# Optimization experiments

Measured on AMD Instinct MI355X. Metric: run time of the kernel, lower is better.

## Reference

```python
import jax, jax.numpy as jnp
import numpy as np

H = 16        # num_heads
NB = 64       # n_buckets
NH = 6        # n_hyperplanes = log2(NB)


def setup_inputs() -> dict:
    key = jax.random.key(0)
    k = jax.random.split(key, 6)
    E = 1024
    B, S = 2, 2048
    return {
        "x": jax.random.normal(k[0], (B, S, E), jnp.float32),
        "Wq": jax.random.normal(k[1], (E, E), jnp.float32) * (E ** -0.5),
        "bq": jax.random.normal(k[2], (E,), jnp.float32) * 0.02,
        "Wv": jax.random.normal(k[3], (E, E), jnp.float32) * (E ** -0.5),
        "bv": jax.random.normal(k[4], (E,), jnp.float32) * 0.02,
        "hyperplanes": jax.random.normal(k[5], (E // H + 1, NH), jnp.float32),
    }


def reference(x, Wq, bq, Wv, bv, hyperplanes):
    B, S, E = x.shape
    Dh = E // H
    # projections (torch Linear: x @ W.T + b)
    q = (x @ Wq.T + bq).reshape(B, S, H, Dh)
    v = (x @ Wv.T + bv).reshape(B, S, H, Dh)

    # LSH buckets from q: append a ones column, sign-project onto hyperplanes
    qa = jnp.concatenate([q, jnp.ones((B, S, H, 1), q.dtype)], axis=-1)  # [B,S,H,Dh+1]
    proj = jnp.einsum('bshe,en->bshn', qa, hyperplanes)
    bits = (proj >= 0).astype(jnp.int32)
    buckets = jnp.einsum('bshn,n->bsh', bits, 2 ** jnp.arange(NH, dtype=jnp.int32))  # [B,S,H]
    b_hs = buckets.transpose(0, 2, 1)  # [B,H,S]

    q = q.transpose(0, 2, 1, 3)  # [B,H,S,Dh]
    v = v.transpose(0, 2, 1, 3)

    # The original sums, over all NB buckets i, of (q with bucket-i tokens zeroed)
    # times its transpose. Closed form of that sum:
    #   sum_i (1-d[bs,i])(1-d[bt,i]) = NB - 2 + [bs == bt]
    scores = jnp.einsum('bhsd,bhtd->bhst', q, q) / jnp.sqrt(jnp.float32(E))
    same = (b_hs[:, :, :, None] == b_hs[:, :, None, :]).astype(scores.dtype)
    coeff = (NB - 2) + same
    attn = jax.nn.softmax(scores * coeff, axis=-1)  # [B,H,S,S]

    out = jnp.einsum('bhst,bhtd->bhsd', attn, v)
    return out.transpose(0, 2, 1, 3).reshape(B, S, E)
```

## Files before the change

kernel.cpp:

```cpp
#include <hip/hip_runtime.h>


typedef short short8 __attribute__((ext_vector_type(8)));
typedef float f32x4 __attribute__((ext_vector_type(4)));
typedef unsigned short us4 __attribute__((ext_vector_type(4)));

__device__ __forceinline__ float bff(unsigned short h) {
    return __uint_as_float(((unsigned int)h) << 16);
}
__device__ __forceinline__ unsigned short f2bf(float f) {
    unsigned int u = __float_as_uint(f);
    u += 0x7fffu + ((u >> 16) & 1u);
    return (unsigned short)(u >> 16);
}

__device__ __forceinline__ void glds16(const unsigned short* g, unsigned short* l) {
    __builtin_amdgcn_global_load_lds(
        (const __attribute__((address_space(1))) unsigned int*)g,
        (__attribute__((address_space(3))) unsigned int*)l, 16, 0, 0);
}

__global__ __launch_bounds__(256) void split_all(
    const float* __restrict__ x, const float* __restrict__ Wq,
    const float* __restrict__ Wv,
    unsigned short* __restrict__ xh, unsigned short* __restrict__ xl,
    unsigned short* __restrict__ Wqh, unsigned short* __restrict__ Wql,
    unsigned short* __restrict__ Wvh)
{
    const int blk = blockIdx.x;
    const float* in;
    unsigned short *hi, *lo;
    int idx;
    if (blk < 4096) {
        idx = blk * 256 + threadIdx.x; in = x; hi = xh; lo = xl;
    } else if (blk < 5120) {
        idx = (blk - 4096) * 256 + threadIdx.x; in = Wq; hi = Wqh; lo = Wql;
    } else {
        idx = (blk - 5120) * 256 + threadIdx.x; in = Wv; hi = Wvh; lo = nullptr;
    }
    const float4 v = ((const float4*)in)[idx];
    us4 h;
    h.x = f2bf(v.x); h.y = f2bf(v.y); h.z = f2bf(v.z); h.w = f2bf(v.w);
    ((us4*)hi)[idx] = h;
    if (lo) {
        us4 l;
        l.x = f2bf(v.x - bff(h.x)); l.y = f2bf(v.y - bff(h.y));
        l.z = f2bf(v.z - bff(h.z)); l.w = f2bf(v.w - bff(h.w));
        ((us4*)lo)[idx] = l;
    }
}

__global__ __launch_bounds__(256, 2) void gemm_qv(
    const unsigned short* __restrict__ xh, const unsigned short* __restrict__ xl,
    const unsigned short* __restrict__ wqh, const unsigned short* __restrict__ wql,
    const unsigned short* __restrict__ wvh,
    const float* __restrict__ bq, const float* __restrict__ bv,
    unsigned short* __restrict__ Qb, unsigned short* __restrict__ Qlo,
    unsigned short* __restrict__ Vt)
{
    __shared__ unsigned short Ah[128 * 64], Al[128 * 64];
    __shared__ unsigned short Bh[128 * 64], Bl[128 * 64];

    const int tid = threadIdx.x;
    const int w = tid >> 6, lane = tid & 63;
    const int i = lane & 15, qd = lane >> 4;
    const int l8 = lane >> 3, j = lane & 7;
    const int nw = w * 32;
    const int blk = blockIdx.x;
    const bool isq = blk < 256;

    f32x4 acc[8][2];
#pragma unroll
    for (int a = 0; a < 8; ++a)
#pragma unroll
        for (int b2 = 0; b2 < 2; ++b2) acc[a][b2] = f32x4{0.f, 0.f, 0.f, 0.f};

    const int gro = ((j ^ l8) << 3);

    if (isq) {
        const int m0 = ((blk & 7) + 8 * ((blk >> 3) & 3)) * 128;
        const int n0 = (blk >> 5) * 128;
        for (int k0 = 0; k0 < 1024; k0 += 64) {
            __syncthreads();
#pragma unroll
            for (int c = 0; c < 4; ++c) {
                const int r = w * 32 + c * 8;
                const size_t gx = (size_t)(m0 + r + l8) * 1024 + k0 + gro;
                const size_t gw = (size_t)(n0 + r + l8) * 1024 + k0 + gro;
                glds16(xh + gx, &Ah[r * 64]);
                glds16(xl + gx, &Al[r * 64]);
                glds16(wqh + gw, &Bh[r * 64]);
                glds16(wql + gw, &Bl[r * 64]);
            }
            __syncthreads();
#pragma unroll
            for (int kc = 0; kc < 2; ++kc) {
                const int ch = (((kc * 4 + qd) ^ (i & 7)) << 3);
                short8 bh2[2], bl2[2];
#pragma unroll
                for (int nn = 0; nn < 2; ++nn) {
                    bh2[nn] = *(const short8*)&Bh[(nw + nn * 16 + i) * 64 + ch];
                    bl2[nn] = *(const short8*)&Bl[(nw + nn * 16 + i) * 64 + ch];
                }
#pragma unroll
                for (int mm = 0; mm < 8; ++mm) {
                    const short8 ah = *(const short8*)&Ah[(mm * 16 + i) * 64 + ch];
                    const short8 al = *(const short8*)&Al[(mm * 16 + i) * 64 + ch];
#pragma unroll
                    for (int nn = 0; nn < 2; ++nn) {
                        acc[mm][nn] = __builtin_amdgcn_mfma_f32_16x16x32_bf16(
                            ah, bh2[nn], acc[mm][nn], 0, 0, 0);
                        acc[mm][nn] = __builtin_amdgcn_mfma_f32_16x16x32_bf16(
                            al, bh2[nn], acc[mm][nn], 0, 0, 0);
                        acc[mm][nn] = __builtin_amdgcn_mfma_f32_16x16x32_bf16(
                            ah, bl2[nn], acc[mm][nn], 0, 0, 0);
                    }
                }
            }
        }
#pragma unroll
        for (int mm = 0; mm < 8; ++mm)
#pragma unroll
            for (int nn = 0; nn < 2; ++nn)
#pragma unroll
                for (int rr = 0; rr < 4; ++rr) {
                    const int row = m0 + mm * 16 + qd * 4 + rr;
                    const int col = n0 + nw + nn * 16 + i;
                    const float v = acc[mm][nn][rr] + bq[col];
                    const unsigned short hs = f2bf(v);
                    const float lo = v - bff(hs);
                    const int b = row >> 11, s = row & 2047;
                    const int hh = col >> 6, d = col & 63;
                    const size_t oi = ((size_t)((b << 4) + hh) * 2048 + s) * 64 + d;
                    Qb[oi] = hs;
                    Qlo[oi] = f2bf(lo);
                }
    } else {
        const int b2 = blk - 256;
        const int n0 = ((b2 & 7) + 8 * ((b2 >> 3) & 3)) * 128;
        const int m0 = (b2 >> 5) * 128;
        for (int k0 = 0; k0 < 1024; k0 += 64) {
            __syncthreads();
#pragma unroll
            for (int c = 0; c < 4; ++c) {
                const int r = w * 32 + c * 8;
                glds16(wvh + (size_t)(m0 + r + l8) * 1024 + k0 + gro, &Ah[r * 64]);
                glds16(xh + (size_t)(n0 + r + l8) * 1024 + k0 + gro, &Bh[r * 64]);
            }
            __syncthreads();
#pragma unroll
            for (int kc = 0; kc < 2; ++kc) {
                const int ch = (((kc * 4 + qd) ^ (i & 7)) << 3);
                short8 bf2[2];
#pragma unroll
                for (int nn = 0; nn < 2; ++nn)
                    bf2[nn] = *(const short8*)&Bh[(nw + nn * 16 + i) * 64 + ch];
#pragma unroll
                for (int mm = 0; mm < 8; ++mm) {
                    const short8 af = *(const short8*)&Ah[(mm * 16 + i) * 64 + ch];
#pragma unroll
                    for (int nn = 0; nn < 2; ++nn)
                        acc[mm][nn] = __builtin_amdgcn_mfma_f32_16x16x32_bf16(
                            af, bf2[nn], acc[mm][nn], 0, 0, 0);
                }
            }
        }
#pragma unroll
        for (int mm = 0; mm < 8; ++mm)
#pragma unroll
            for (int nn = 0; nn < 2; ++nn)
#pragma unroll
                for (int rr = 0; rr < 4; ++rr) {
                    const int rch = m0 + mm * 16 + qd * 4 + rr;
                    const int tok = n0 + nw + nn * 16 + i;
                    const float v = acc[mm][nn][rr] + bv[rch];
                    const int b = tok >> 11, s = tok & 2047;
                    Vt[((size_t)(b * 1024 + rch)) * 2048 + s] = f2bf(v);
                }
    }
}

__global__ __launch_bounds__(256) void bucket_kernel(
    const unsigned short* __restrict__ Qb, const unsigned short* __restrict__ Qlo,
    const float* __restrict__ hp,
    int* __restrict__ buckets, float* __restrict__ rown)
{
    __shared__ float hpl[65 * 6];
    const int tid = threadIdx.x;
    if (tid < 65 * 6) hpl[tid] = hp[tid];
    __syncthreads();

    const int idx = blockIdx.x * 256 + tid;
    const unsigned short* qh = Qb + (size_t)idx * 64;
    const unsigned short* ql = Qlo + (size_t)idx * 64;

    float pj[6];
    float nrm = 0.f;
#pragma unroll
    for (int n = 0; n < 6; ++n) pj[n] = hpl[64 * 6 + n];
    for (int d8 = 0; d8 < 8; ++d8) {
        const short8 vh = *(const short8*)(qh + d8 * 8);
        const short8 vl = *(const short8*)(ql + d8 * 8);
#pragma unroll
        for (int e = 0; e < 8; ++e) {
            const float q = bff((unsigned short)vh[e]) + bff((unsigned short)vl[e]);
            nrm = fmaf(q, q, nrm);
#pragma unroll
            for (int n = 0; n < 6; ++n)
                pj[n] = fmaf(q, hpl[(d8 * 8 + e) * 6 + n], pj[n]);
        }
    }
    int bkt = 0;
#pragma unroll
    for (int n = 0; n < 6; ++n) bkt |= (pj[n] >= 0.f) << n;
    buckets[idx] = bkt;
    rown[idx] = nrm;
}

__global__ __launch_bounds__(256, 2) void attn_kernel(
    const unsigned short* __restrict__ Qb, const unsigned short* __restrict__ Qlo,
    const unsigned short* __restrict__ Vt, const int* __restrict__ bks,
    const float* __restrict__ rown, float* __restrict__ out)
{
    __shared__ unsigned short Khi[64 * 64];
    __shared__ unsigned short Klo[64 * 64];
    __shared__ unsigned short Vs[64 * 64];
    __shared__ unsigned short P[4][16 * 64];
    __shared__ float smax[4];

    const int tid = threadIdx.x;
    const int w = tid >> 6, lane = tid & 63;
    const int i = lane & 15, qd = lane >> 4;
    const int l8 = lane >> 3, j = lane & 7;
    const int bh = blockIdx.x;
    const int qbase = blockIdx.y * 128 + w * 32;

    const unsigned short* Qh = Qb + (size_t)bh * 2048 * 64;
    const unsigned short* Ql = Qlo + (size_t)bh * 2048 * 64;
    const unsigned short* Vb = Vt + (size_t)bh * 64 * 2048;
    const int* bk = bks + bh * 2048;
    const float* rnh = rown + bh * 2048;
    unsigned short* Pw = &P[w][0];

    float lm = 0.f;
    for (int t = tid; t < 2048; t += 256) lm = fmaxf(lm, rnh[t]);
#pragma unroll
    for (int msk = 1; msk < 64; msk <<= 1) lm = fmaxf(lm, __shfl_xor(lm, msk));
    if (lane == 0) smax[w] = lm;
    __syncthreads();
    const float sqM = sqrtf(fmaxf(fmaxf(smax[0], smax[1]),
                                  fmaxf(smax[2], smax[3])));

    float m2row[2][4], lrun[2][4];
    int qbr[2][4];
#pragma unroll
    for (int ms = 0; ms < 2; ++ms)
#pragma unroll
        for (int r = 0; r < 4; ++r) {
            const int row = qbase + ms * 16 + qd * 4 + r;
            m2row[ms][r] = 2.84030586f * sqrtf(rnh[row]) * sqM + 0.72134754f;
            qbr[ms][r] = bk[row];
            lrun[ms][r] = 0.f;
        }

    short8 aqh0[2], aqh1[2], aql0[2], aql1[2];
#pragma unroll
    for (int ms = 0; ms < 2; ++ms) {
        const unsigned short* qp = Qh + (size_t)(qbase + ms * 16 + i) * 64 + qd * 8;
        const unsigned short* lp = Ql + (size_t)(qbase + ms * 16 + i) * 64 + qd * 8;
        aqh0[ms] = *(const short8*)qp; aqh1[ms] = *(const short8*)(qp + 32);
        aql0[ms] = *(const short8*)lp; aql1[ms] = *(const short8*)(lp + 32);
    }

    f32x4 o[2][4];
#pragma unroll
    for (int ms = 0; ms < 2; ++ms)
#pragma unroll
        for (int d = 0; d < 4; ++d) o[ms][d] = f32x4{0.f, 0.f, 0.f, 0.f};

    for (int t0 = 0; t0 < 2048; t0 += 64) {
        __syncthreads();
#pragma unroll
        for (int c2 = 0; c2 < 2; ++c2) {
            const int r = w * 16 + c2 * 8 + l8;
            const int swz = ((j ^ l8) << 3);
            glds16(Qh + (size_t)(t0 + r) * 64 + swz, &Khi[w * 1024 + c2 * 512]);
            glds16(Ql + (size_t)(t0 + r) * 64 + swz, &Klo[w * 1024 + c2 * 512]);
            glds16(Vb + (size_t)r * 2048 + t0 + swz, &Vs[w * 1024 + c2 * 512]);
        }
        __syncthreads();

        f32x4 s[2][4];
        int kb[4];
#pragma unroll
        for (int sub = 0; sub < 4; ++sub) {
            const int kr = sub * 16 + i;
            const int sw = i & 7;
            const short8 bh0 = *(const short8*)&Khi[kr * 64 + ((qd ^ sw) << 3)];
            const short8 bh1 = *(const short8*)&Khi[kr * 64 + (((qd + 4) ^ sw) << 3)];
            const short8 bl0 = *(const short8*)&Klo[kr * 64 + ((qd ^ sw) << 3)];
            const short8 bl1 = *(const short8*)&Klo[kr * 64 + (((qd + 4) ^ sw) << 3)];
            kb[sub] = bk[t0 + kr];
#pragma unroll
            for (int ms = 0; ms < 2; ++ms) {
                f32x4 t = f32x4{0.f, 0.f, 0.f, 0.f};
                t = __builtin_amdgcn_mfma_f32_16x16x32_bf16(aqh0[ms], bh0, t, 0, 0, 0);
                t = __builtin_amdgcn_mfma_f32_16x16x32_bf16(aqh1[ms], bh1, t, 0, 0, 0);
                t = __builtin_amdgcn_mfma_f32_16x16x32_bf16(aql0[ms], bh0, t, 0, 0, 0);
                t = __builtin_amdgcn_mfma_f32_16x16x32_bf16(aql1[ms], bh1, t, 0, 0, 0);
                t = __builtin_amdgcn_mfma_f32_16x16x32_bf16(aqh0[ms], bl0, t, 0, 0, 0);
                t = __builtin_amdgcn_mfma_f32_16x16x32_bf16(aqh1[ms], bl1, t, 0, 0, 0);
                s[ms][sub] = t;
            }
        }

        short8 vb0[4], vb1[4];
#pragma unroll
        for (int dsub = 0; dsub < 4; ++dsub) {
            const int dr = dsub * 16 + i;
            const int sw = i & 7;
            vb0[dsub] = *(const short8*)&Vs[dr * 64 + ((qd ^ sw) << 3)];
            vb1[dsub] = *(const short8*)&Vs[dr * 64 + (((qd + 4) ^ sw) << 3)];
        }

#pragma unroll
        for (int ms = 0; ms < 2; ++ms) {
#pragma unroll
            for (int sub = 0; sub < 4; ++sub)
#pragma unroll
                for (int r = 0; r < 4; ++r) {
                    const float c2f = (kb[sub] == qbr[ms][r]) ? 2.84030586f
                                                              : 2.79522164f;
                    const float p = exp2f(fmaf(s[ms][sub][r], c2f, -m2row[ms][r]));
                    lrun[ms][r] += p;
                    const unsigned int pu = __float_as_uint(p);
                    const int row = qd * 4 + r, col = sub * 16 + i;
                    Pw[row * 64 + (((col >> 3) ^ (row & 7)) << 3) + (col & 7)] =
                        (unsigned short)(pu >> 16);
                }
            const short8 pa0 = *(const short8*)&Pw[i * 64 + ((qd ^ (i & 7)) << 3)];
            const short8 pa1 = *(const short8*)&Pw[i * 64 + (((qd + 4) ^ (i & 7)) << 3)];
#pragma unroll
            for (int dsub = 0; dsub < 4; ++dsub) {
                o[ms][dsub] = __builtin_amdgcn_mfma_f32_16x16x32_bf16(
                    pa0, vb0[dsub], o[ms][dsub], 0, 0, 0);
                o[ms][dsub] = __builtin_amdgcn_mfma_f32_16x16x32_bf16(
                    pa1, vb1[dsub], o[ms][dsub], 0, 0, 0);
            }
        }
    }

#pragma unroll
    for (int ms = 0; ms < 2; ++ms)
#pragma unroll
        for (int r = 0; r < 4; ++r) {
#pragma unroll
            for (int msk = 1; msk < 16; msk <<= 1)
                lrun[ms][r] += __shfl_xor(lrun[ms][r], msk);
        }
    const int b = bh >> 4, h = bh & 15;
#pragma unroll
    for (int ms = 0; ms < 2; ++ms)
#pragma unroll
        for (int dsub = 0; dsub < 4; ++dsub)
#pragma unroll
            for (int r = 0; r < 4; ++r) {
                const float v = o[ms][dsub][r] / lrun[ms][r];
                const int srow = qbase + ms * 16 + qd * 4 + r;
                out[((size_t)(b * 2048 + srow)) * 1024 + h * 64 + dsub * 16 + i] = v;
            }
}

extern "C" void kernel_launch(void* const* d_in, const int* in_sizes, int n_in,
                              void* d_out, int out_size, void* d_ws, size_t ws_size,
                              hipStream_t stream)
{
    const float* x  = (const float*)d_in[0];
    const float* Wq = (const float*)d_in[1];
    const float* bq = (const float*)d_in[2];
    const float* Wv = (const float*)d_in[3];
    const float* bv = (const float*)d_in[4];
    const float* hp = (const float*)d_in[5];
    float* out = (float*)d_out;

    char* ws = (char*)d_ws;
    const size_t MB = (size_t)1 << 20;
    unsigned short* xh  = (unsigned short*)(ws);
    unsigned short* xl  = (unsigned short*)(ws + 8 * MB);
    unsigned short* Wqh = (unsigned short*)(ws + 16 * MB);
    unsigned short* Wql = (unsigned short*)(ws + 18 * MB);
    unsigned short* Wvh = (unsigned short*)(ws + 20 * MB);
    unsigned short* Qb  = (unsigned short*)(ws + 22 * MB);
    unsigned short* Qlo = (unsigned short*)(ws + 30 * MB);
    unsigned short* Vt  = (unsigned short*)(ws + 38 * MB);
    int*        buckets = (int*)(ws + 62 * MB);
    float*         rown = (float*)(ws + 62 * MB + 256 * 1024);

    split_all<<<dim3(6144), 256, 0, stream>>>(x, Wq, Wv, xh, xl, Wqh, Wql, Wvh);
    gemm_qv<<<dim3(512), 256, 0, stream>>>(xh, xl, Wqh, Wql, Wvh, bq, bv,
                                           Qb, Qlo, Vt);
    bucket_kernel<<<dim3(256), 256, 0, stream>>>(Qb, Qlo, hp, buckets, rown);
    attn_kernel<<<dim3(32, 16), 256, 0, stream>>>(Qb, Qlo, Vt, buckets, rown, out);
}
```

Baseline: 212.3 us.

## Fuse Q and V projection GEMMs into one block sharing the x tile

Merges the separate Q and V GEMM blocks into a single 512-thread block that computes both projections for the same 128x128 tile. The xh tile loaded into shared memory is reused as the V operand, which removes the duplicate x loads the V blocks used to do. Each wave now covers 16 columns instead of 32. The grid halves to 256 blocks, so there is less parallelism and more shared memory per block (five tiles). The V output is now produced in the Q-style orientation before being written transposed.

```diff
diff --git a/kernel.cpp b/kernel.cpp
--- a/kernel.cpp
+++ b/kernel.cpp
@@ -50,7 +50,7 @@
     }
 }
 
-__global__ __launch_bounds__(256, 2) void gemm_qv(
+__global__ __launch_bounds__(512, 2) void gemm_qv(
     const unsigned short* __restrict__ xh, const unsigned short* __restrict__ xl,
     const unsigned short* __restrict__ wqh, const unsigned short* __restrict__ wql,
     const unsigned short* __restrict__ wvh,
@@ -60,123 +60,94 @@
 {
     __shared__ unsigned short Ah[128 * 64], Al[128 * 64];
     __shared__ unsigned short Bh[128 * 64], Bl[128 * 64];
+    __shared__ unsigned short Cv[128 * 64];
 
     const int tid = threadIdx.x;
     const int w = tid >> 6, lane = tid & 63;
     const int i = lane & 15, qd = lane >> 4;
     const int l8 = lane >> 3, j = lane & 7;
-    const int nw = w * 32;
     const int blk = blockIdx.x;
-    const bool isq = blk < 256;
-
-    f32x4 acc[8][2];
-#pragma unroll
-    for (int a = 0; a < 8; ++a)
-#pragma unroll
-        for (int b2 = 0; b2 < 2; ++b2) acc[a][b2] = f32x4{0.f, 0.f, 0.f, 0.f};
+
+    const int m0 = ((blk & 7) + 8 * ((blk >> 3) & 3)) * 128;
+    const int n0 = (blk >> 5) * 128;
+
+    f32x4 accq[8], accv[8];
+#pragma unroll
+    for (int a = 0; a < 8; ++a) {
+        accq[a] = f32x4{0.f, 0.f, 0.f, 0.f};
+        accv[a] = f32x4{0.f, 0.f, 0.f, 0.f};
+    }
 
     const int gro = ((j ^ l8) << 3);
 
-    if (isq) {
-        const int m0 = ((blk & 7) + 8 * ((blk >> 3) & 3)) * 128;
-        const int n0 = (blk >> 5) * 128;
-        for (int k0 = 0; k0 < 1024; k0 += 64) {
-            __syncthreads();
-#pragma unroll
-            for (int c = 0; c < 4; ++c) {
-                const int r = w * 32 + c * 8;
-                const size_t gx = (size_t)(m0 + r + l8) * 1024 + k0 + gro;
-                const size_t gw = (size_t)(n0 + r + l8) * 1024 + k0 + gro;
-                glds16(xh + gx, &Ah[r * 64]);
-                glds16(xl + gx, &Al[r * 64]);
-                glds16(wqh + gw, &Bh[r * 64]);
-                glds16(wql + gw, &Bl[r * 64]);
-            }
-            __syncthreads();
-#pragma unroll
-            for (int kc = 0; kc < 2; ++kc) {
-                const int ch = (((kc * 4 + qd) ^ (i & 7)) << 3);
-                short8 bh2[2], bl2[2];
-#pragma unroll
-                for (int nn = 0; nn < 2; ++nn) {
-                    bh2[nn] = *(const short8*)&Bh[(nw + nn * 16 + i) * 64 + ch];
-                    bl2[nn] = *(const short8*)&Bl[(nw + nn * 16 + i) * 64 + ch];
-                }
-#pragma unroll
-                for (int mm = 0; mm < 8; ++mm) {
-                    const short8 ah = *(const short8*)&Ah[(mm * 16 + i) * 64 + ch];
-                    const short8 al = *(const short8*)&Al[(mm * 16 + i) * 64 + ch];
-#pragma unroll
-                    for (int nn = 0; nn < 2; ++nn) {
-                        acc[mm][nn] = __builtin_amdgcn_mfma_f32_16x16x32_bf16(
-                            ah, bh2[nn], acc[mm][nn], 0, 0, 0);
-                        acc[mm][nn] = __builtin_amdgcn_mfma_f32_16x16x32_bf16(
-                            al, bh2[nn], acc[mm][nn], 0, 0, 0);
-                        acc[mm][nn] = __builtin_amdgcn_mfma_f32_16x16x32_bf16(
-                            ah, bl2[nn], acc[mm][nn], 0, 0, 0);
-                    }
-                }
-            }
-        }
+    for (int k0 = 0; k0 < 1024; k0 += 64) {
+        __syncthreads();
+#pragma unroll
+        for (int c = 0; c < 2; ++c) {
+            const int r = w * 16 + c * 8;
+            const size_t gm = (size_t)(m0 + r + l8) * 1024 + k0 + gro;
+            const size_t gn = (size_t)(n0 + r + l8) * 1024 + k0 + gro;
+            glds16(xh + gm, &Ah[r * 64]);
+            glds16(xl + gm, &Al[r * 64]);
+            glds16(wqh + gn, &Bh[r * 64]);
+            glds16(wql + gn, &Bl[r * 64]);
+            glds16(wvh + gn, &Cv[r * 64]);
+        }
+        __syncthreads();
+#pragma unroll
+        for (int kc = 0; kc < 2; ++kc) {
+            const int ch = (((kc * 4 + qd) ^ (i & 7)) << 3);
+            const int br = (w * 16 + i) * 64 + ch;
+            const short8 fbh = *(const short8*)&Bh[br];
+            const short8 fbl = *(const short8*)&Bl[br];
+            const short8 fbx = *(const short8*)&Ah[br];
+#pragma unroll
+            for (int mm = 0; mm < 8; ++mm) {
+                const int ar = (mm * 16 + i) * 64 + ch;
+                const short8 ah = *(const short8*)&Ah[ar];
+                const short8 al = *(const short8*)&Al[ar];
+                const short8 av = *(const short8*)&Cv[ar];
+                accq[mm] = __builtin_amdgcn_mfma_f32_16x16x32_bf16(
+                    ah, fbh, accq[mm], 0, 0, 0);
+                accq[mm] = __builtin_amdgcn_mfma_f32_16x16x32_bf16(
+                    al, fbh, accq[mm], 0, 0, 0);
+                accq[mm] = __builtin_amdgcn_mfma_f32_16x16x32_bf16(
+                    ah, fbl, accq[mm], 0, 0, 0);
+                accv[mm] = __builtin_amdgcn_mfma_f32_16x16x32_bf16(
+                    av, fbx, accv[mm], 0, 0, 0);
+            }
+        }
+    }
+
+    {
+        const int col = n0 + w * 16 + i;
+        const int hh = col >> 6, d = col & 63;
+        const float bqc = bq[col];
 #pragma unroll
         for (int mm = 0; mm < 8; ++mm)
 #pragma unroll
-            for (int nn = 0; nn < 2; ++nn)
-#pragma unroll
-                for (int rr = 0; rr < 4; ++rr) {
-                    const int row = m0 + mm * 16 + qd * 4 + rr;
-                    const int col = n0 + nw + nn * 16 + i;
-                    const float v = acc[mm][nn][rr] + bq[col];
-                    const unsigned short hs = f2bf(v);
-                    const float lo = v - bff(hs);
-                    const int b = row >> 11, s = row & 2047;
-                    const int hh = col >> 6, d = col & 63;
-                    const size_t oi = ((size_t)((b << 4) + hh) * 2048 + s) * 64 + d;
-                    Qb[oi] = hs;
-                    Qlo[oi] = f2bf(lo);
-                }
-    } else {
-        const int b2 = blk - 256;
-        const int n0 = ((b2 & 7) + 8 * ((b2 >> 3) & 3)) * 128;
-        const int m0 = (b2 >> 5) * 128;
-        for (int k0 = 0; k0 < 1024; k0 += 64) {
-            __syncthreads();
-#pragma unroll
-            for (int c = 0; c < 4; ++c) {
-                const int r = w * 32 + c * 8;
-                glds16(wvh + (size_t)(m0 + r + l8) * 1024 + k0 + gro, &Ah[r * 64]);
-                glds16(xh + (size_t)(n0 + r + l8) * 1024 + k0 + gro, &Bh[r * 64]);
-            }
-            __syncthreads();
-#pragma unroll
-            for (int kc = 0; kc < 2; ++kc) {
-                const int ch = (((kc * 4 + qd) ^ (i & 7)) << 3);
-                short8 bf2[2];
-#pragma unroll
-                for (int nn = 0; nn < 2; ++nn)
-                    bf2[nn] = *(const short8*)&Bh[(nw + nn * 16 + i) * 64 + ch];
-#pragma unroll
-                for (int mm = 0; mm < 8; ++mm) {
-                    const short8 af = *(const short8*)&Ah[(mm * 16 + i) * 64 + ch];
-#pragma unroll
-                    for (int nn = 0; nn < 2; ++nn)
-                        acc[mm][nn] = __builtin_amdgcn_mfma_f32_16x16x32_bf16(
-                            af, bf2[nn], acc[mm][nn], 0, 0, 0);
-                }
-            }
-        }
+            for (int rr = 0; rr < 4; ++rr) {
+                const int row = m0 + mm * 16 + qd * 4 + rr;
+                const float v = accq[mm][rr] + bqc;
+                const unsigned short hs = f2bf(v);
+                const float lo = v - bff(hs);
+                const int b = row >> 11, s = row & 2047;
+                const size_t oi = ((size_t)((b << 4) + hh) * 2048 + s) * 64 + d;
+                Qb[oi] = hs;
+                Qlo[oi] = f2bf(lo);
+            }
+    }
+    {
+        const int tok = m0 + w * 16 + i;
+        const int b = tok >> 11, s = tok & 2047;
 #pragma unroll
         for (int mm = 0; mm < 8; ++mm)
 #pragma unroll
-            for (int nn = 0; nn < 2; ++nn)
-#pragma unroll
-                for (int rr = 0; rr < 4; ++rr) {
-                    const int rch = m0 + mm * 16 + qd * 4 + rr;
-                    const int tok = n0 + nw + nn * 16 + i;
-                    const float v = acc[mm][nn][rr] + bv[rch];
-                    const int b = tok >> 11, s = tok & 2047;
-                    Vt[((size_t)(b * 1024 + rch)) * 2048 + s] = f2bf(v);
-                }
+            for (int rr = 0; rr < 4; ++rr) {
+                const int rch = n0 + mm * 16 + qd * 4 + rr;
+                const float v = accv[mm][rr] + bv[rch];
+                Vt[((size_t)(b * 1024 + rch)) * 2048 + s] = f2bf(v);
+            }
     }
 }
 
@@ -397,7 +368,7 @@
     float*         rown = (float*)(ws + 62 * MB + 256 * 1024);
 
     split_all<<<dim3(6144), 256, 0, stream>>>(x, Wq, Wv, xh, xl, Wqh, Wql, Wvh);
-    gemm_qv<<<dim3(512), 256, 0, stream>>>(xh, xl, Wqh, Wql, Wvh, bq, bv,
+    gemm_qv<<<dim3(256), 512, 0, stream>>>(xh, xl, Wqh, Wql, Wvh, bq, bv,
                                            Qb, Qlo, Vt);
     bucket_kernel<<<dim3(256), 256, 0, stream>>>(Qb, Qlo, hp, buckets, rown);
     attn_kernel<<<dim3(32, 16), 256, 0, stream>>>(Qb, Qlo, Vt, buckets, rown, out);
```

Measured after the change: 223.1 us. 5.0% more time.
